# Kernel tuning notes

Measured on AMD Instinct MI355X. Metric: run time of the kernel, lower is better.

## Reference

```python
import jax, jax.numpy as jnp
import numpy as np

ETYPES = ((0, 2), (4, 6))  # per-metapath edge-type indices into the doubled r_vec table
ALPHA = 3.0


def celu3(x):
    return jax.nn.celu(x, alpha=ALPHA)


def cmul(a, b):
    # complex multiply, last dim = (real, imag)
    re = a[..., 0] * b[..., 0] - a[..., 1] * b[..., 1]
    im = a[..., 0] * b[..., 1] + a[..., 1] * b[..., 0]
    return jnp.stack([re, im], axis=-1)


def setup_inputs() -> dict:
    key = jax.random.key(0)
    ks = jax.random.split(key, 10)
    N, H, heads, M, E, P = 50000, 64, 4, 2, 250000, 3
    R, FH = 4, 128
    D = heads * H
    return {
        "features": jax.random.normal(ks[0], (N, H), jnp.float32),
        "r_vec": jax.random.normal(ks[1], (R, H // 2, 2), jnp.float32),
        "attn1_w": jax.random.normal(ks[2], (heads, H), jnp.float32) * 0.1,
        "attn2": jax.random.normal(ks[3], (1, heads, H), jnp.float32) * 0.1,
        "fw1": jax.random.normal(ks[4], (2 * FH, D), jnp.float32) * 0.05,
        "fb1": jnp.zeros((2 * FH,), jnp.float32),
        "fw2": jax.random.normal(ks[5], (FH, 2 * FH), jnp.float32) * 0.05,
        "fb2": jnp.zeros((FH,), jnp.float32),
        "fw3": jax.random.normal(ks[6], (1, FH), jnp.float32) * 0.05,
        "instances": jax.random.randint(ks[7], (M, E, P), 0, N, jnp.int32),
    }


def reference(features, r_vec, attn1_w, attn2, fw1, fb1, fw2, fb2, fw3, instances):
    N, H = features.shape
    M, E, P = instances.shape
    heads = attn1_w.shape[0]
    # unit-modulus rotations + conjugates: [2R, H/2, 2], even=r, odd=conj(r)
    rv = r_vec / jnp.linalg.norm(r_vec, axis=2, keepdims=True)
    conj = rv * jnp.array([1.0, -1.0], rv.dtype)
    rv2 = jnp.stack([rv, conj], axis=1).reshape(-1, H // 2, 2)

    per_path = []
    for m in range(M):
        inst = instances[m]  # [E, P]
        # backward cumulative rotation: final_r[i] = prod_{j>=i} r_{etype[j]}, final_r[P-1]=1
        ident = jnp.stack([jnp.ones(H // 2, rv.dtype), jnp.zeros(H // 2, rv.dtype)], axis=-1)
        frs = [ident]
        for i in range(P - 2, -1, -1):
            frs.insert(0, cmul(frs[0], rv2[ETYPES[m][i]]))
        fr = jnp.stack(frs)  # [P, H/2, 2]
        # gather features along metapath and rotate (last position rotated by identity)
        edata = features[inst].reshape(E, P, H // 2, 2)
        rot = cmul(edata, fr[None])
        me = jnp.mean(rot.reshape(E, P, H), axis=1)  # [E, H]
        se = celu3(me) * jax.nn.sigmoid(me)  # gated metapath embedding
        eft = celu3(se)  # same across heads in original (tiled)
        seg = inst[:, 0]  # target node per instance
        a1 = celu3(features[seg] @ attn1_w.T)  # [E, heads]
        a2 = jnp.einsum('eh,kh->ek', eft, attn2[0])  # [E, heads]
        a = celu3(a1 + a2)
        # segment softmax over each node's instance set
        amax = jax.ops.segment_max(a, seg, num_segments=N)
        ex = jnp.exp(a - amax[seg])
        den = jax.ops.segment_sum(ex, seg, num_segments=N)
        attn = ex / den[seg]  # [E, heads]
        hsum = jax.ops.segment_sum(attn[:, :, None] * eft[:, None, :], seg, num_segments=N)
        per_path.append(celu3(hsum).reshape(N, heads * H))  # empty nodes -> 0

    z = jnp.stack(per_path, axis=1)  # [N, M, D]
    t = celu3(z @ fw1.T + fb1)
    t = celu3(t @ fw2.T + fb2)
    w = (t @ fw3.T).mean(axis=0)  # [M, 1]
    beta = jax.nn.softmax(w, axis=0)
    out = (beta * z).sum(axis=1)  # [N, D]
    return out
```

## Files before the change

kernel.cpp:

```cpp
#include <hip/hip_runtime.h>
#include <hip/hip_bf16.h>

typedef unsigned short u16;
typedef unsigned int   u32;
typedef short bf16x8 __attribute__((ext_vector_type(8)));
typedef float f32x4  __attribute__((ext_vector_type(4)));

#define CAP 64

__device__ inline float b2f(u16 u){ return __builtin_bit_cast(float, (u32)u << 16); }
__device__ inline u16 f2b(float f){
  u32 x = __builtin_bit_cast(u32, f);
  x += 0x7fffu + ((x >> 16) & 1u);
  return (u16)(x >> 16);
}
__device__ inline u32 pk2(float lo, float hi){
  float2 f; f.x = lo; f.y = hi;
  __hip_bfloat162 h = __float22bfloat162_rn(f);
  u32 r; __builtin_memcpy(&r, &h, 4);
  return r;
}
__device__ inline void up2(u32 u, float& lo, float& hi){
  lo = __builtin_bit_cast(float, u << 16);
  hi = __builtin_bit_cast(float, u & 0xffff0000u);
}
__device__ inline float fexp(float x){ return __expf(x); }
__device__ inline float frcp(float x){ return __builtin_amdgcn_rcpf(x); }
__device__ inline float celu3(float x){
  return x > 0.f ? x : 3.f * (__expf(x * (1.f/3.f)) - 1.f);
}
__device__ inline float act_chain(float x){
  float u  = __expf(x * (1.f/3.f));
  float u3 = u*u*u;
  float sg = u3 * frcp(u3 + 1.f);
  float c1 = x > 0.f ? x : 3.f*u - 3.f;
  float se = c1 * sg;
  return se > 0.f ? se : 3.f*__expf(se*(1.f/3.f)) - 3.f;
}

__global__ __launch_bounds__(256) void pre_kernel(
    const float* __restrict__ feat, const float* __restrict__ attn1,
    const float* __restrict__ rvec, const float* __restrict__ fw1,
    const float* __restrict__ fw2,
    u16* __restrict__ featb, u16* __restrict__ rotA, u16* __restrict__ rotB,
    float* __restrict__ a1c, u16* __restrict__ fw1b, u16* __restrict__ fw2b,
    int N, int nbA)
{
  __shared__ float w1s[256], rvs[256];
  int b = blockIdx.x, t = threadIdx.x;
  if (b >= nbA){
    int cb = b - nbA;
    const float* src = (cb < 32) ? fw1 : fw2;
    u16* dst = (cb < 32) ? fw1b : fw2b;
    int i = (cb < 32 ? cb : cb - 32)*256 + t;
    float4 a = ((const float4*)src)[2*i], bb = ((const float4*)src)[2*i + 1];
    uint4 o;
    o.x = pk2(a.x, a.y);  o.y = pk2(a.z, a.w);
    o.z = pk2(bb.x, bb.y); o.w = pk2(bb.z, bb.w);
    ((uint4*)dst)[i] = o;
    return;
  }
  w1s[t] = attn1[t];
  rvs[t] = rvec[t];
  __syncthreads();
  int g = t >> 4, l = t & 15;
  int n = b * 16 + g;
  if (n >= N) return;
  float4 x = ((const float4*)feat)[(size_t)n*16 + l];
  uint2 o;
  o.x = pk2(x.x, x.y);
  o.y = pk2(x.z, x.w);
  ((uint2*)featb)[(size_t)n*16 + l] = o;

  #pragma unroll
  for (int m = 0; m < 2; ++m){
    float4 ra = *(const float4*)&rvs[(2*m)*64 + l*4];
    float4 rb = *(const float4*)&rvs[(2*m+1)*64 + l*4];
    float na0 = rsqrtf(ra.x*ra.x + ra.y*ra.y); ra.x*=na0; ra.y*=na0;
    float na1 = rsqrtf(ra.z*ra.z + ra.w*ra.w); ra.z*=na1; ra.w*=na1;
    float nb0 = rsqrtf(rb.x*rb.x + rb.y*rb.y); rb.x*=nb0; rb.y*=nb0;
    float nb1 = rsqrtf(rb.z*rb.z + rb.w*rb.w); rb.z*=nb1; rb.w*=nb1;
    float A0r = rb.x*ra.x - rb.y*ra.y, A0i = rb.x*ra.y + rb.y*ra.x;
    float A1r = rb.z*ra.z - rb.w*ra.w, A1i = rb.z*ra.w + rb.w*ra.z;
    uint2 oa, ob;
    oa.x = pk2(x.x*A0r - x.y*A0i, x.x*A0i + x.y*A0r);
    oa.y = pk2(x.z*A1r - x.w*A1i, x.z*A1i + x.w*A1r);
    ob.x = pk2(x.x*rb.x - x.y*rb.y, x.x*rb.y + x.y*rb.x);
    ob.y = pk2(x.z*rb.z - x.w*rb.w, x.z*rb.w + x.w*rb.z);
    ((uint2*)rotA)[((size_t)m*N + n)*16 + l] = oa;
    ((uint2*)rotB)[((size_t)m*N + n)*16 + l] = ob;
  }

  float d[4];
  #pragma unroll
  for (int k = 0; k < 4; ++k){
    int wb = k*64 + l*4;
    d[k] = x.x*w1s[wb] + x.y*w1s[wb+1] + x.z*w1s[wb+2] + x.w*w1s[wb+3];
  }
  #pragma unroll
  for (int off = 8; off; off >>= 1){
    #pragma unroll
    for (int k = 0; k < 4; ++k) d[k] += __shfl_xor(d[k], off);
  }
  if (l == 0){
    float4 av;
    av.x = celu3(d[0]); av.y = celu3(d[1]);
    av.z = celu3(d[2]); av.w = celu3(d[3]);
    ((float4*)a1c)[n] = av;
  }
}

__global__ __launch_bounds__(256) void edge_kernel(
    const u16* __restrict__ rotA, const u16* __restrict__ rotB,
    const u16* __restrict__ featb, const int* __restrict__ inst,
    const float* __restrict__ a1c, const float* __restrict__ attn2,
    u16* __restrict__ eft, float* __restrict__ a_ws,
    int* __restrict__ cnt, int* __restrict__ bucket, int E, int N)
{
  __shared__ float w2s[256];
  int m = blockIdx.y;
  int t = threadIdx.x;
  w2s[t] = attn2[t];
  __syncthreads();

  int g = t >> 4, l = t & 15;
  int e = blockIdx.x * 16 + g;
  if (e >= E) return;
  int base = (m*E + e)*3;
  int i0 = inst[base], i1 = inst[base+1], i2 = inst[base+2];
  size_t mN = (size_t)m * N;

  uint2 v0 = ((const uint2*)rotA)[(mN + i0)*16 + l];
  uint2 v1 = ((const uint2*)rotB)[(mN + i1)*16 + l];
  uint2 v2 = ((const uint2*)featb)[(size_t)i2*16 + l];
  float a0,a1v,a2v,a3, b0,b1,b2,b3, c0,c1,c2,c3;
  up2(v0.x, a0, a1v); up2(v0.y, a2v, a3);
  up2(v1.x, b0, b1);  up2(v1.y, b2, b3);
  up2(v2.x, c0, c1);  up2(v2.y, c2, c3);

  float ef[4];
  ef[0] = act_chain((a0 + b0 + c0) * (1.f/3.f));
  ef[1] = act_chain((a1v + b1 + c1) * (1.f/3.f));
  ef[2] = act_chain((a2v + b2 + c2) * (1.f/3.f));
  ef[3] = act_chain((a3 + b3 + c3) * (1.f/3.f));

  uint2 uo;
  uo.x = pk2(ef[0], ef[1]);
  uo.y = pk2(ef[2], ef[3]);
  ((uint2*)eft)[(size_t)(m*E + e)*16 + l] = uo;

  float d2[4];
  #pragma unroll
  for (int k = 0; k < 4; ++k){
    int wb = k*64 + l*4;
    d2[k] = ef[0]*w2s[wb] + ef[1]*w2s[wb+1] + ef[2]*w2s[wb+2] + ef[3]*w2s[wb+3];
  }
  #pragma unroll
  for (int off = 8; off; off >>= 1){
    #pragma unroll
    for (int k = 0; k < 4; ++k) d2[k] += __shfl_xor(d2[k], off);
  }
  if (l == 0){
    float4 a1v4 = ((const float4*)a1c)[i0];
    float4 av;
    av.x = celu3(a1v4.x + d2[0]);
    av.y = celu3(a1v4.y + d2[1]);
    av.z = celu3(a1v4.z + d2[2]);
    av.w = celu3(a1v4.w + d2[3]);
    ((float4*)a_ws)[m*E + e] = av;
    int pos = atomicAdd(&cnt[m*N + i0], 1);
    if (pos < CAP) bucket[(size_t)(m*N + i0)*CAP + pos] = e;
  }
}

__global__ __launch_bounds__(256) void seg_kernel(
    const float* __restrict__ a_ws, const u16* __restrict__ eft,
    const int* __restrict__ cnt, const int* __restrict__ bucket,
    u16* __restrict__ z, int E, int N)
{
  __shared__ float wls[4][64][4];
  __shared__ int   els[4][64];
  int wvb = threadIdx.x >> 6;
  int m = blockIdx.y;
  int n = blockIdx.x * 4 + wvb;
  if (n >= N) return;
  int lane = threadIdx.x & 63;
  int sidx = m*N + n;
  int deg = cnt[sidx]; if (deg > CAP) deg = CAP;

  float h0=0.f, h1=0.f, h2=0.f, h3=0.f;
  if (deg > 0){
    const int* bk = bucket + (size_t)sidx * CAP;
    size_t ebase = (size_t)m * E;

    int e = (lane < deg) ? bk[lane] : 0;
    float w0 = 0.f, w1 = 0.f, w2 = 0.f, w3 = 0.f;
    if (lane < deg){
      float4 av = ((const float4*)a_ws)[ebase + e];
      w0 = fexp(av.x); w1 = fexp(av.y); w2 = fexp(av.z); w3 = fexp(av.w);
    }
    els[wvb][lane] = e;
    *(float4*)&wls[wvb][lane][0] = make_float4(w0, w1, w2, w3);

    float d0=w0, d1=w1, d2=w2, d3=w3;
    #pragma unroll
    for (int off = 32; off; off >>= 1){
      d0 += __shfl_xor(d0, off); d1 += __shfl_xor(d1, off);
      d2 += __shfl_xor(d2, off); d3 += __shfl_xor(d3, off);
    }

    const u16* ep = eft + ebase*64 + lane;
    int j = 0;
    for (; j + 1 < deg; j += 2){
      int ej0 = els[wvb][j], ej1 = els[wvb][j+1];
      float4 wj0 = *(const float4*)&wls[wvb][j][0];
      float4 wj1 = *(const float4*)&wls[wvb][j+1][0];
      float ev0 = b2f(ep[(size_t)ej0*64]);
      float ev1 = b2f(ep[(size_t)ej1*64]);
      h0 += wj0.x*ev0; h1 += wj0.y*ev0; h2 += wj0.z*ev0; h3 += wj0.w*ev0;
      h0 += wj1.x*ev1; h1 += wj1.y*ev1; h2 += wj1.z*ev1; h3 += wj1.w*ev1;
    }
    if (j < deg){
      int ej0 = els[wvb][j];
      float4 wj0 = *(const float4*)&wls[wvb][j][0];
      float ev0 = b2f(ep[(size_t)ej0*64]);
      h0 += wj0.x*ev0; h1 += wj0.y*ev0; h2 += wj0.z*ev0; h3 += wj0.w*ev0;
    }
    h0 *= frcp(d0); h1 *= frcp(d1); h2 *= frcp(d2); h3 *= frcp(d3);
  }
  u16* zr = z + (size_t)sidx*256 + lane;
  zr[0]   = f2b(celu3(h0));
  zr[64]  = f2b(celu3(h1));
  zr[128] = f2b(celu3(h2));
  zr[192] = f2b(celu3(h3));
}

__global__ __launch_bounds__(512, 4) void mlp_kernel(
    const u16* __restrict__ z, const u16* __restrict__ fw1b, const float* __restrict__ fb1,
    const u16* __restrict__ fw2b, const float* __restrict__ fb2, const float* __restrict__ fw3,
    float* __restrict__ waccP, int rows, int N)
{
  __shared__ u16 buf[64][264];
  __shared__ float fw3s[128];
  __shared__ float sPart[8][64];
  int tid = threadIdx.x;
  int row0 = blockIdx.x * 64;
  int wv = tid >> 6, lane = tid & 63, lr = lane & 15, quad = lane >> 4;

  const uint4* zg = (const uint4*)z;
  uint4 zr4[4];
  #pragma unroll
  for (int it = 0; it < 4; ++it){
    int idx = it*512 + tid;
    int row = idx >> 5, c8 = idx & 31;
    int gr = row0 + row;
    zr4[it] = make_uint4(0u,0u,0u,0u);
    if (gr < rows) zr4[it] = zg[(size_t)gr*32 + c8];
  }

  const u16* wb1 = fw1b + (size_t)(wv*32 + lr)*256 + quad*8;
  bf16x8 B1[2][8];
  #pragma unroll
  for (int nt = 0; nt < 2; ++nt)
    #pragma unroll
    for (int ks = 0; ks < 8; ++ks)
      B1[nt][ks] = *(const bf16x8*)(wb1 + nt*16*256 + ks*32);

  if (tid < 128) fw3s[tid] = fw3[tid];

  #pragma unroll
  for (int it = 0; it < 4; ++it){
    int idx = it*512 + tid;
    int row = idx >> 5, c8 = idx & 31;
    *(uint4*)&buf[row][c8*8] = zr4[it];
  }
  __syncthreads();

  f32x4 zero4 = {0.f, 0.f, 0.f, 0.f};

  f32x4 acc[4][2];
  #pragma unroll
  for (int a = 0; a < 4; ++a){ acc[a][0] = zero4; acc[a][1] = zero4; }
  #pragma unroll
  for (int ks = 0; ks < 8; ++ks){
    #pragma unroll
    for (int mt = 0; mt < 4; ++mt){
      bf16x8 af = *(const bf16x8*)&buf[mt*16 + lr][ks*32 + quad*8];
      acc[mt][0] = __builtin_amdgcn_mfma_f32_16x16x32_bf16(af, B1[0][ks], acc[mt][0], 0, 0, 0);
      acc[mt][1] = __builtin_amdgcn_mfma_f32_16x16x32_bf16(af, B1[1][ks], acc[mt][1], 0, 0, 0);
    }
  }

  const u16* wb2 = fw2b + (size_t)(wv*16 + lr)*256 + quad*8;
  bf16x8 B2[8];
  #pragma unroll
  for (int ks = 0; ks < 8; ++ks)
    B2[ks] = *(const bf16x8*)(wb2 + ks*32);

  __syncthreads();
  #pragma unroll
  for (int nt = 0; nt < 2; ++nt){
    int col = wv*32 + nt*16 + lr;
    float bias = fb1[col];
    #pragma unroll
    for (int mt = 0; mt < 4; ++mt)
      #pragma unroll
      for (int ri = 0; ri < 4; ++ri){
        int row = mt*16 + quad*4 + ri;
        buf[row][col] = f2b(celu3(acc[mt][nt][ri] + bias));
      }
  }
  __syncthreads();

  f32x4 acc2[4];
  #pragma unroll
  for (int a = 0; a < 4; ++a) acc2[a] = zero4;
  #pragma unroll
  for (int ks = 0; ks < 8; ++ks){
    #pragma unroll
    for (int mt = 0; mt < 4; ++mt){
      bf16x8 af = *(const bf16x8*)&buf[mt*16 + lr][ks*32 + quad*8];
      acc2[mt] = __builtin_amdgcn_mfma_f32_16x16x32_bf16(af, B2[ks], acc2[mt], 0, 0, 0);
    }
  }

  {
    int col = wv*16 + lr;
    float bias2 = fb2[col];
    float w3 = fw3s[col];
    float ps[4][4];
    #pragma unroll
    for (int mt = 0; mt < 4; ++mt)
      #pragma unroll
      for (int ri = 0; ri < 4; ++ri)
        ps[mt][ri] = celu3(acc2[mt][ri] + bias2) * w3;
    #pragma unroll
    for (int off = 8; off; off >>= 1)
      #pragma unroll
      for (int mt = 0; mt < 4; ++mt)
        #pragma unroll
        for (int ri = 0; ri < 4; ++ri)
          ps[mt][ri] += __shfl_xor(ps[mt][ri], off);
    if (lr == 0){
      #pragma unroll
      for (int mt = 0; mt < 4; ++mt)
        #pragma unroll
        for (int ri = 0; ri < 4; ++ri)
          sPart[wv][mt*16 + quad*4 + ri] = ps[mt][ri];
    }
  }
  __syncthreads();

  if (tid < 64){
    float s = 0.f;
    #pragma unroll
    for (int w = 0; w < 8; ++w) s += sPart[w][tid];
    int gr = row0 + tid;
    if (gr >= rows) s = 0.f;
    float s0 = (gr < N) ? s : 0.f;
    float s1 = (gr < N) ? 0.f : s;
    #pragma unroll
    for (int off = 32; off; off >>= 1){
      s0 += __shfl_xor(s0, off);
      s1 += __shfl_xor(s1, off);
    }
    if (tid == 0){
      int slot = blockIdx.x & 63;
      atomicAdd(&waccP[slot],      s0);
      atomicAdd(&waccP[64 + slot], s1);
    }
  }
}

__global__ void beta_kernel(float* __restrict__ wacc, float invN){
  int t = threadIdx.x;
  float s0 = wacc[t], s1 = wacc[64 + t];
  #pragma unroll
  for (int off = 32; off; off >>= 1){
    s0 += __shfl_xor(s0, off);
    s1 += __shfl_xor(s1, off);
  }
  if (t == 0){
    float w0 = s0*invN, w1 = s1*invN;
    float mx = fmaxf(w0, w1);
    float e0 = __expf(w0 - mx), e1 = __expf(w1 - mx);
    float s = e0 + e1;
    wacc[128] = e0 / s;
    wacc[129] = e1 / s;
  }
}

__global__ __launch_bounds__(256) void out_kernel(
    const u16* __restrict__ z, const float* __restrict__ wacc,
    float* __restrict__ out, int total)
{
  int idx = blockIdx.x * 256 + threadIdx.x;
  if (idx*8 >= total) return;
  float b0 = wacc[128], b1 = wacc[129];
  uint4 u0 = ((const uint4*)z)[idx];
  uint4 u1 = ((const uint4*)z)[(total >> 3) + idx];
  float a0,a1v,c0,c1;
  float4 o;
  up2(u0.x, a0, a1v); up2(u1.x, c0, c1);
  o.x = b0*a0 + b1*c0; o.y = b0*a1v + b1*c1;
  up2(u0.y, a0, a1v); up2(u1.y, c0, c1);
  o.z = b0*a0 + b1*c0; o.w = b0*a1v + b1*c1;
  ((float4*)out)[idx*2] = o;
  up2(u0.z, a0, a1v); up2(u1.z, c0, c1);
  o.x = b0*a0 + b1*c0; o.y = b0*a1v + b1*c1;
  up2(u0.w, a0, a1v); up2(u1.w, c0, c1);
  o.z = b0*a0 + b1*c0; o.w = b0*a1v + b1*c1;
  ((float4*)out)[idx*2 + 1] = o;
}

extern "C" void kernel_launch(void* const* d_in, const int* in_sizes, int n_in,
                              void* d_out, int out_size, void* d_ws, size_t ws_size,
                              hipStream_t stream)
{
  (void)n_in; (void)out_size; (void)ws_size;
  const float* feat  = (const float*)d_in[0];
  const float* rvec  = (const float*)d_in[1];
  const float* attn1 = (const float*)d_in[2];
  const float* attn2 = (const float*)d_in[3];
  const float* fw1   = (const float*)d_in[4];
  const float* fb1   = (const float*)d_in[5];
  const float* fw2   = (const float*)d_in[6];
  const float* fb2   = (const float*)d_in[7];
  const float* fw3   = (const float*)d_in[8];
  const int*   inst  = (const int*)d_in[9];

  int N = in_sizes[0] / 64;
  int E = in_sizes[9] / 6;

  char* ws = (char*)d_ws;
  u16*   z      = (u16*)ws;                            size_t zB = (size_t)2*N*256*2;
  u16*   eft    = (u16*)(ws + zB);                     size_t eB = (size_t)2*E*64*2;
  float* a_ws   = (float*)(ws + zB + eB);              size_t aB = (size_t)2*E*4*4;
  int*   bucket = (int*)(ws + zB + eB + aB);           size_t bB = (size_t)2*N*CAP*4;
  int*   cnt    = (int*)(ws + zB + eB + aB + bB);      size_t cB = (size_t)2*N*4;
  u16*   featb  = (u16*)(ws + zB + eB + aB + bB + cB); size_t fB = (size_t)N*64*2;
  float* a1c    = (float*)(ws + zB + eB + aB + bB + cB + fB);  size_t a1B = (size_t)N*4*4;
  u16*   fw1b   = (u16*)(ws + zB + eB + aB + bB + cB + fB + a1B);
  u16*   fw2b   = fw1b + 256*256;
  float* wacc   = (float*)(fw2b + 128*256);

  u16* rotA = z;
  u16* rotB = z + (size_t)2*N*64;

  hipMemsetAsync(cnt, 0, cB, stream);
  hipMemsetAsync(wacc, 0, 128*sizeof(float), stream);

  int nbA = (N + 15)/16;
  pre_kernel<<<nbA + 48, 256, 0, stream>>>(
      feat, attn1, rvec, fw1, fw2, featb, rotA, rotB, a1c, fw1b, fw2b, N, nbA);
  edge_kernel<<<dim3((E + 15)/16, 2), 256, 0, stream>>>(
      rotA, rotB, featb, inst, a1c, attn2, eft, a_ws, cnt, bucket, E, N);
  seg_kernel<<<dim3((N + 3)/4, 2), 256, 0, stream>>>(a_ws, eft, cnt, bucket, z, E, N);
  mlp_kernel<<<(2*N + 63)/64, 512, 0, stream>>>(z, fw1b, fb1, fw2b, fb2, fw3, wacc, 2*N, N);
  beta_kernel<<<1, 64, 0, stream>>>(wacc, 1.f/(float)N);
  out_kernel<<<((N*256/8) + 255)/256, 256, 0, stream>>>(z, wacc, (float*)d_out, N*256);
}
```

Baseline: 273.6 us.

## Fold memsets and beta kernel into neighbors; widen edge gather to 8 lanes

The cnt/wacc zeroing moves from two hipMemsetAsync calls into extra blocks of pre_kernel, and the beta softmax is recomputed redundantly in every out_kernel block, removing three launches. The 1/3 mean scale is folded into the precomputed rotated and bf16 features. edge_kernel now uses 8 lanes per edge with 16-byte loads and stores, giving wider memory transactions and a shorter shuffle reduction. The trade-offs are redundant beta work in each out block and higher register pressure in edge_kernel.

```diff
diff --git a/kernel.cpp b/kernel.cpp
--- a/kernel.cpp
+++ b/kernel.cpp
@@ -44,20 +44,28 @@
     const float* __restrict__ fw2,
     u16* __restrict__ featb, u16* __restrict__ rotA, u16* __restrict__ rotB,
     float* __restrict__ a1c, u16* __restrict__ fw1b, u16* __restrict__ fw2b,
+    int* __restrict__ cnt, float* __restrict__ wacc,
     int N, int nbA)
 {
   __shared__ float w1s[256], rvs[256];
   int b = blockIdx.x, t = threadIdx.x;
   if (b >= nbA){
     int cb = b - nbA;
-    const float* src = (cb < 32) ? fw1 : fw2;
-    u16* dst = (cb < 32) ? fw1b : fw2b;
-    int i = (cb < 32 ? cb : cb - 32)*256 + t;
-    float4 a = ((const float4*)src)[2*i], bb = ((const float4*)src)[2*i + 1];
-    uint4 o;
-    o.x = pk2(a.x, a.y);  o.y = pk2(a.z, a.w);
-    o.z = pk2(bb.x, bb.y); o.w = pk2(bb.z, bb.w);
-    ((uint4*)dst)[i] = o;
+    if (cb < 48){
+      const float* src = (cb < 32) ? fw1 : fw2;
+      u16* dst = (cb < 32) ? fw1b : fw2b;
+      int i = (cb < 32 ? cb : cb - 32)*256 + t;
+      float4 a = ((const float4*)src)[2*i], bb = ((const float4*)src)[2*i + 1];
+      uint4 o;
+      o.x = pk2(a.x, a.y);  o.y = pk2(a.z, a.w);
+      o.z = pk2(bb.x, bb.y); o.w = pk2(bb.z, bb.w);
+      ((uint4*)dst)[i] = o;
+      return;
+    }
+    cb -= 48;
+    int i = cb*256 + t;
+    if (i*4 < 2*N) ((uint4*)cnt)[i] = make_uint4(0u,0u,0u,0u);
+    if (cb == 0 && t < 128) wacc[t] = 0.f;
     return;
   }
   w1s[t] = attn1[t];
@@ -67,9 +75,12 @@
   int n = b * 16 + g;
   if (n >= N) return;
   float4 x = ((const float4*)feat)[(size_t)n*16 + l];
+  float4 xs;
+  xs.x = x.x*(1.f/3.f); xs.y = x.y*(1.f/3.f);
+  xs.z = x.z*(1.f/3.f); xs.w = x.w*(1.f/3.f);
   uint2 o;
-  o.x = pk2(x.x, x.y);
-  o.y = pk2(x.z, x.w);
+  o.x = pk2(xs.x, xs.y);
+  o.y = pk2(xs.z, xs.w);
   ((uint2*)featb)[(size_t)n*16 + l] = o;
 
   #pragma unroll
@@ -83,10 +94,10 @@
     float A0r = rb.x*ra.x - rb.y*ra.y, A0i = rb.x*ra.y + rb.y*ra.x;
     float A1r = rb.z*ra.z - rb.w*ra.w, A1i = rb.z*ra.w + rb.w*ra.z;
     uint2 oa, ob;
-    oa.x = pk2(x.x*A0r - x.y*A0i, x.x*A0i + x.y*A0r);
-    oa.y = pk2(x.z*A1r - x.w*A1i, x.z*A1i + x.w*A1r);
-    ob.x = pk2(x.x*rb.x - x.y*rb.y, x.x*rb.y + x.y*rb.x);
-    ob.y = pk2(x.z*rb.z - x.w*rb.w, x.z*rb.w + x.w*rb.z);
+    oa.x = pk2(xs.x*A0r - xs.y*A0i, xs.x*A0i + xs.y*A0r);
+    oa.y = pk2(xs.z*A1r - xs.w*A1i, xs.z*A1i + xs.w*A1r);
+    ob.x = pk2(xs.x*rb.x - xs.y*rb.y, xs.x*rb.y + xs.y*rb.x);
+    ob.y = pk2(xs.z*rb.z - xs.w*rb.w, xs.z*rb.w + xs.w*rb.z);
     ((uint2*)rotA)[((size_t)m*N + n)*16 + l] = oa;
     ((uint2*)rotB)[((size_t)m*N + n)*16 + l] = ob;
   }
@@ -123,40 +134,47 @@
   w2s[t] = attn2[t];
   __syncthreads();
 
-  int g = t >> 4, l = t & 15;
-  int e = blockIdx.x * 16 + g;
+  int g = t >> 3, l = t & 7;
+  int e = blockIdx.x * 32 + g;
   if (e >= E) return;
   int base = (m*E + e)*3;
   int i0 = inst[base], i1 = inst[base+1], i2 = inst[base+2];
   size_t mN = (size_t)m * N;
 
-  uint2 v0 = ((const uint2*)rotA)[(mN + i0)*16 + l];
-  uint2 v1 = ((const uint2*)rotB)[(mN + i1)*16 + l];
-  uint2 v2 = ((const uint2*)featb)[(size_t)i2*16 + l];
-  float a0,a1v,a2v,a3, b0,b1,b2,b3, c0,c1,c2,c3;
-  up2(v0.x, a0, a1v); up2(v0.y, a2v, a3);
-  up2(v1.x, b0, b1);  up2(v1.y, b2, b3);
-  up2(v2.x, c0, c1);  up2(v2.y, c2, c3);
-
-  float ef[4];
-  ef[0] = act_chain((a0 + b0 + c0) * (1.f/3.f));
-  ef[1] = act_chain((a1v + b1 + c1) * (1.f/3.f));
-  ef[2] = act_chain((a2v + b2 + c2) * (1.f/3.f));
-  ef[3] = act_chain((a3 + b3 + c3) * (1.f/3.f));
-
-  uint2 uo;
+  uint4 v0 = ((const uint4*)rotA)[(mN + i0)*8 + l];
+  uint4 v1 = ((const uint4*)rotB)[(mN + i1)*8 + l];
+  uint4 v2 = ((const uint4*)featb)[(size_t)i2*8 + l];
+  float A[8], B[8], C[8];
+  up2(v0.x, A[0], A[1]); up2(v0.y, A[2], A[3]);
+  up2(v0.z, A[4], A[5]); up2(v0.w, A[6], A[7]);
+  up2(v1.x, B[0], B[1]); up2(v1.y, B[2], B[3]);
+  up2(v1.z, B[4], B[5]); up2(v1.w, B[6], B[7]);
+  up2(v2.x, C[0], C[1]); up2(v2.y, C[2], C[3]);
+  up2(v2.z, C[4], C[5]); up2(v2.w, C[6], C[7]);
+
+  float ef[8];
+  #pragma unroll
+  for (int c = 0; c < 8; ++c)
+    ef[c] = act_chain(A[c] + B[c] + C[c]);
+
+  uint4 uo;
   uo.x = pk2(ef[0], ef[1]);
   uo.y = pk2(ef[2], ef[3]);
-  ((uint2*)eft)[(size_t)(m*E + e)*16 + l] = uo;
+  uo.z = pk2(ef[4], ef[5]);
+  uo.w = pk2(ef[6], ef[7]);
+  ((uint4*)eft)[(size_t)(m*E + e)*8 + l] = uo;
 
   float d2[4];
   #pragma unroll
   for (int k = 0; k < 4; ++k){
-    int wb = k*64 + l*4;
-    d2[k] = ef[0]*w2s[wb] + ef[1]*w2s[wb+1] + ef[2]*w2s[wb+2] + ef[3]*w2s[wb+3];
-  }
-  #pragma unroll
-  for (int off = 8; off; off >>= 1){
+    int wb = k*64 + l*8;
+    float4 wA = *(const float4*)&w2s[wb];
+    float4 wB = *(const float4*)&w2s[wb+4];
+    d2[k] = ef[0]*wA.x + ef[1]*wA.y + ef[2]*wA.z + ef[3]*wA.w
+          + ef[4]*wB.x + ef[5]*wB.y + ef[6]*wB.z + ef[7]*wB.w;
+  }
+  #pragma unroll
+  for (int off = 4; off; off >>= 1){
     #pragma unroll
     for (int k = 0; k < 4; ++k) d2[k] += __shfl_xor(d2[k], off);
   }
@@ -372,31 +390,32 @@
   }
 }
 
-__global__ void beta_kernel(float* __restrict__ wacc, float invN){
-  int t = threadIdx.x;
-  float s0 = wacc[t], s1 = wacc[64 + t];
-  #pragma unroll
-  for (int off = 32; off; off >>= 1){
-    s0 += __shfl_xor(s0, off);
-    s1 += __shfl_xor(s1, off);
-  }
-  if (t == 0){
-    float w0 = s0*invN, w1 = s1*invN;
-    float mx = fmaxf(w0, w1);
-    float e0 = __expf(w0 - mx), e1 = __expf(w1 - mx);
-    float s = e0 + e1;
-    wacc[128] = e0 / s;
-    wacc[129] = e1 / s;
-  }
-}
-
 __global__ __launch_bounds__(256) void out_kernel(
     const u16* __restrict__ z, const float* __restrict__ wacc,
-    float* __restrict__ out, int total)
-{
-  int idx = blockIdx.x * 256 + threadIdx.x;
+    float* __restrict__ out, int total, float invN)
+{
+  __shared__ float bsh[2];
+  int tid = threadIdx.x;
+  if (tid < 64){
+    float s0 = wacc[tid], s1 = wacc[64 + tid];
+    #pragma unroll
+    for (int off = 32; off; off >>= 1){
+      s0 += __shfl_xor(s0, off);
+      s1 += __shfl_xor(s1, off);
+    }
+    if (tid == 0){
+      float w0 = s0*invN, w1 = s1*invN;
+      float mx = fmaxf(w0, w1);
+      float e0 = __expf(w0 - mx), e1 = __expf(w1 - mx);
+      float s = e0 + e1;
+      bsh[0] = e0 / s;
+      bsh[1] = e1 / s;
+    }
+  }
+  __syncthreads();
+  float b0 = bsh[0], b1 = bsh[1];
+  int idx = blockIdx.x * 256 + tid;
   if (idx*8 >= total) return;
-  float b0 = wacc[128], b1 = wacc[129];
   uint4 u0 = ((const uint4*)z)[idx];
   uint4 u1 = ((const uint4*)z)[(total >> 3) + idx];
   float a0,a1v,c0,c1;
@@ -447,16 +466,14 @@
   u16* rotA = z;
   u16* rotB = z + (size_t)2*N*64;
 
-  hipMemsetAsync(cnt, 0, cB, stream);
-  hipMemsetAsync(wacc, 0, 128*sizeof(float), stream);
-
   int nbA = (N + 15)/16;
-  pre_kernel<<<nbA + 48, 256, 0, stream>>>(
-      feat, attn1, rvec, fw1, fw2, featb, rotA, rotB, a1c, fw1b, fw2b, N, nbA);
-  edge_kernel<<<dim3((E + 15)/16, 2), 256, 0, stream>>>(
+  int nbZ = ((2*N)/4 + 255)/256;
+  pre_kernel<<<nbA + 48 + nbZ, 256, 0, stream>>>(
+      feat, attn1, rvec, fw1, fw2, featb, rotA, rotB, a1c, fw1b, fw2b,
+      cnt, wacc, N, nbA);
+  edge_kernel<<<dim3((E + 31)/32, 2), 256, 0, stream>>>(
       rotA, rotB, featb, inst, a1c, attn2, eft, a_ws, cnt, bucket, E, N);
   seg_kernel<<<dim3((N + 3)/4, 2), 256, 0, stream>>>(a_ws, eft, cnt, bucket, z, E, N);
   mlp_kernel<<<(2*N + 63)/64, 512, 0, stream>>>(z, fw1b, fb1, fw2b, fb2, fw3, wacc, 2*N, N);
-  beta_kernel<<<1, 64, 0, stream>>>(wacc, 1.f/(float)N);
-  out_kernel<<<((N*256/8) + 255)/256, 256, 0, stream>>>(z, wacc, (float*)d_out, N*256);
-}
+  out_kernel<<<((N*256/8) + 255)/256, 256, 0, stream>>>(z, wacc, (float*)d_out, N*256, 1.f/(float)N);
+}
```

Result: no change. 270.9 us (-1.0%).
